# Optimization experiments

Measured on AMD Instinct MI355X. Metric: run time of the kernel, lower is better.

The kernel has to match this reference:

```python
import jax, jax.numpy as jnp
import numpy as np

INNER_STEPS = 50
INNER_LR = 0.1
Y_MEAN = 0.0


def _mlp(params, inp):
    # eqx.nn.MLP(in=3, out=1, width=64, depth=3): relu hidden, identity final
    W1, b1, W2, b2, W3, b3, W4, b4 = params
    h = jax.nn.relu(W1 @ inp + b1)
    h = jax.nn.relu(W2 @ h + b2)
    h = jax.nn.relu(W3 @ h + b3)
    return jnp.squeeze(W4 @ h + b4)


def setup_inputs() -> dict:
    key = jax.random.key(0)
    ks = jax.random.split(key, 10)
    B, CD, W = 8192, 1, 64
    d_in = 2 + CD
    x = jax.random.normal(ks[0], (B, 1), dtype=jnp.float32)
    c = jax.random.normal(ks[1], (B, CD), dtype=jnp.float32)
    def lin(k, fan_out, fan_in):
        lim = 1.0 / np.sqrt(fan_in)
        kw, kb = jax.random.split(k)
        Wm = jax.random.uniform(kw, (fan_out, fan_in), minval=-lim, maxval=lim, dtype=jnp.float32)
        bm = jax.random.uniform(kb, (fan_out,), minval=-lim, maxval=lim, dtype=jnp.float32)
        return Wm, bm
    W1, b1 = lin(ks[2], W, d_in)
    W2, b2 = lin(ks[3], W, W)
    W3, b3 = lin(ks[4], W, W)
    W4, b4 = lin(ks[5], 1, W)
    return {"x": x, "c": c, "W1": W1, "b1": b1, "W2": W2, "b2": b2,
            "W3": W3, "b3": b3, "W4": W4, "b4": b4}


def reference(x, c, W1, b1, W2, b2, W3, b3, W4, b4):
    params = (W1, b1, W2, b2, W3, b3, W4, b4)
    # nearest-neighbor c0 per sample (excluding self)
    dists = jnp.linalg.norm(c[:, None, :] - c[None, :, :], axis=-1)  # [B,B]
    dists = dists + jnp.eye(dists.shape[0], dtype=dists.dtype) * 1e9
    c0 = c[jnp.argmin(dists, axis=1)]  # [B,CD]

    def base_energy(xi, yi, ci):
        return _mlp(params, jnp.concatenate([xi, yi, ci], axis=0))

    def solve(xi, ci, c0i):
        y0 = jnp.array([Y_MEAN], dtype=xi.dtype)

        def step(y, _):
            def loss(yy):
                E0, dE = jax.jvp(lambda cc: base_energy(xi, yy, cc), (c0i,), (ci - c0i,))
                return E0 + dE
            gy = jax.grad(loss)(y)
            return y - INNER_LR * gy, None

        yf, _ = jax.lax.scan(step, y0, None, length=INNER_STEPS)
        return yf

    return jax.vmap(solve)(x, c, c0)  # [B,1]
```

## Files before the change

kernel.cpp:

```cpp
#include <hip/hip_runtime.h>

#define BATCH 8192
#define LOSC  2048.0f
#define LOINV (1.0f / 2048.0f)

typedef _Float16 f16x8 __attribute__((ext_vector_type(8)));
typedef __fp16   fp16x2 __attribute__((ext_vector_type(2)));
typedef float    f32x4 __attribute__((ext_vector_type(4)));

union PK2 { fp16x2 h; unsigned u; };
union U8  { f16x8 v; unsigned u[4]; };

#define FWDMASK 0x00FF00FF00FF00FFULL

__device__ __forceinline__ unsigned pkrtz(float a, float b) {
    PK2 p; p.h = __builtin_amdgcn_cvt_pkrtz(a, b); return p.u;
}

__device__ __forceinline__ unsigned lopair(unsigned hipk, float am, float bm,
                                           float n2048) {
    unsigned d;
    asm("v_fma_mixlo_f16 %0, %1, %2, %3 op_sel:[0,0,0] op_sel_hi:[1,0,0]\n\t"
        "v_fma_mixhi_f16 %0, %1, %2, %4 op_sel:[1,0,0] op_sel_hi:[1,0,0]"
        : "=&v"(d)
        : "v"(hipk), "v"(n2048), "v"(am), "v"(bm));
    return d;
}

__device__ __forceinline__ float xor8f(float v) {
    const int r = __builtin_amdgcn_mov_dpp(__builtin_bit_cast(int, v),
                                           0x128 , 0xf, 0xf, false);
    return __builtin_bit_cast(float, r);
}

__device__ __forceinline__ float selmask(float v, unsigned long long m) {
    float r;
    asm("v_cndmask_b32 %0, 0, %1, %2" : "=v"(r) : "v"(v), "s"(m));
    return r;
}

__device__ __forceinline__ float bfly16(float g) {
    float a = g, b;
    asm volatile("v_mov_b32 %0, %1" : "=v"(b) : "v"(g));
    asm("v_permlane16_swap_b32 %0, %1" : "+v"(a), "+v"(b));
    return a + b;
}
__device__ __forceinline__ float bfly32(float g) {
    float a = g, b;
    asm volatile("v_mov_b32 %0, %1" : "=v"(b) : "v"(g));
    asm("v_permlane32_swap_b32 %0, %1" : "+v"(a), "+v"(b));
    return a + b;
}

__global__ __launch_bounds__(64, 1) void solve_kernel(
    const float* __restrict__ x, const float* __restrict__ c,
    const float* __restrict__ W1, const float* __restrict__ b1,
    const float* __restrict__ W2, const float* __restrict__ b2,
    const float* __restrict__ W3, const float* __restrict__ b3,
    const float* __restrict__ W4, float* __restrict__ out)
{
    const int lane  = threadIdx.x & 63;
    const int sbase = blockIdx.x * 8;
    const float n2048 = -2048.0f;

    __shared__ float cs[BATCH];
    {
        const float4* cg = (const float4*)c;
        float4* cl = (float4*)cs;
        #pragma unroll
        for (int j = 0; j < BATCH / 4 / 64; ++j)
            cl[lane + j * 64] = cg[lane + j * 64];
    }
    __syncthreads();

    float c0s;
    {
        const int g  = lane >> 3;
        const int p  = lane & 7;
        const int si = sbase + g;
        const float ci = cs[si];
        const int sj0 = ((si & 3) == 0) ? (si >> 2) : -1;
        const int sj1 = ((si & 3) == 1) ? (si >> 2) : -1;
        const int sj2 = ((si & 3) == 2) ? (si >> 2) : -1;
        const int sj3 = ((si & 3) == 3) ? (si >> 2) : -1;
        const float4* cs4 = (const float4*)cs;
        float bd0 = 3e38f, bd1 = 3e38f, bd2 = 3e38f, bd3 = 3e38f;
        int   bj0 = 0,     bj1 = 0,     bj2 = 0,     bj3 = 0;
        #pragma unroll 1
        for (int big = 0; big < 16; ++big) {
            float4 vv[16];
            #pragma unroll
            for (int u = 0; u < 16; ++u)
                vv[u] = cs4[p + (big * 16 + u) * 8];
            #pragma unroll
            for (int u = 0; u < 16; ++u) {
                const int jj = p + (big * 16 + u) * 8;
                const float4 v = vv[u];
                float d0 = fabsf(ci - v.x);
                float d1 = fabsf(ci - v.y);
                float d2 = fabsf(ci - v.z);
                float d3 = fabsf(ci - v.w);
                if (jj == sj0) d0 = 3e38f;
                if (jj == sj1) d1 = 3e38f;
                if (jj == sj2) d2 = 3e38f;
                if (jj == sj3) d3 = 3e38f;
                if (d0 < bd0) { bd0 = d0; bj0 = jj; }
                if (d1 < bd1) { bd1 = d1; bj1 = jj; }
                if (d2 < bd2) { bd2 = d2; bj2 = jj; }
                if (d3 < bd3) { bd3 = d3; bj3 = jj; }
            }
        }
        float best = bd0; int bestj = bj0 * 4 + 0;
        { const int j1 = bj1 * 4 + 1; if (bd1 < best || (bd1 == best && j1 < bestj)) { best = bd1; bestj = j1; } }
        { const int j2 = bj2 * 4 + 2; if (bd2 < best || (bd2 == best && j2 < bestj)) { best = bd2; bestj = j2; } }
        { const int j3 = bj3 * 4 + 3; if (bd3 < best || (bd3 == best && j3 < bestj)) { best = bd3; bestj = j3; } }
        #pragma unroll
        for (int off = 1; off < 8; off <<= 1) {
            const float od = __shfl_xor(best, off);
            const int   oj = __shfl_xor(bestj, off);
            if (od < best || (od == best && oj < bestj)) { best = od; bestj = oj; }
        }
        const float bestc = cs[bestj];
        c0s = __shfl(bestc, (lane & 7) << 3);
    }

    const int q  = lane >> 4;
    const int cc = lane & 15;
    const bool fwd = (cc < 8);
    const int s = cc & 7;

    f16x8 W2h[4][2], W2l[4][2], W3h[4][2], W3l[4][2];
    #pragma unroll
    for (int T = 0; T < 4; ++T)
        #pragma unroll
        for (int M = 0; M < 2; ++M) {
            const int off0 = (T * 16 + cc) * 64 + M * 32 + q * 4;
            const int off1 = off0 + 16;
            float4 a = *(const float4*)(W2 + off0);
            float4 b = *(const float4*)(W2 + off1);
            U8 h, l;
            h.u[0] = pkrtz(a.x, a.y); h.u[1] = pkrtz(a.z, a.w);
            h.u[2] = pkrtz(b.x, b.y); h.u[3] = pkrtz(b.z, b.w);
            l.u[0] = lopair(h.u[0], a.x * LOSC, a.y * LOSC, n2048);
            l.u[1] = lopair(h.u[1], a.z * LOSC, a.w * LOSC, n2048);
            l.u[2] = lopair(h.u[2], b.x * LOSC, b.y * LOSC, n2048);
            l.u[3] = lopair(h.u[3], b.z * LOSC, b.w * LOSC, n2048);
            W2h[T][M] = h.v; W2l[T][M] = l.v;
            a = *(const float4*)(W3 + off0);
            b = *(const float4*)(W3 + off1);
            h.u[0] = pkrtz(a.x, a.y); h.u[1] = pkrtz(a.z, a.w);
            h.u[2] = pkrtz(b.x, b.y); h.u[3] = pkrtz(b.z, b.w);
            l.u[0] = lopair(h.u[0], a.x * LOSC, a.y * LOSC, n2048);
            l.u[1] = lopair(h.u[1], a.z * LOSC, a.w * LOSC, n2048);
            l.u[2] = lopair(h.u[2], b.x * LOSC, b.y * LOSC, n2048);
            l.u[3] = lopair(h.u[3], b.z * LOSC, b.w * LOSC, n2048);
            W3h[T][M] = h.v; W3l[T][M] = l.v;
        }

    f32x4 b2q[4], b3q[4];
    const f32x4 zq = {0.f, 0.f, 0.f, 0.f};
    float w4r[16];
    #pragma unroll
    for (int T = 0; T < 4; ++T)
        #pragma unroll
        for (int r = 0; r < 4; ++r) {
            const int row = T * 16 + q * 4 + r;
            b2q[T][r] = fwd ? b2[row] : 0.f;
            b3q[T][r] = fwd ? b3[row] : 0.f;
            w4r[T * 4 + r] = W4[row];
        }

    float A1v[16], w11v[16];
    {
        const float xs = x[sbase + s];
        #pragma unroll
        for (int m = 0; m < 4; ++m)
            #pragma unroll
            for (int j = 0; j < 4; ++j) {
                const int k = m * 16 + q * 4 + j;
                w11v[m * 4 + j] = W1[k * 3 + 1];
                A1v[m * 4 + j]  = fmaf(xs, W1[k * 3 + 0],
                                       fmaf(c0s, W1[k * 3 + 2], b1[k]));
            }
    }

    float y = 0.0f;

    #pragma unroll 1
    for (int step = 0; step < 50; ++step) {
        U8 B1h[2], B1l[2];
        #pragma unroll
        for (int m = 0; m < 4; ++m) {
            float v[4];
            #pragma unroll
            for (int j = 0; j < 4; ++j) {
                const float w = w11v[m * 4 + j];
                const float z = fmaf(y, w, A1v[m * 4 + j]);
                const float a = fwd ? z : w;
                v[j] = (z > 0.f) ? a : 0.f;
            }
            const unsigned h0 = pkrtz(v[0], v[1]);
            const unsigned h1 = pkrtz(v[2], v[3]);
            const int M = m >> 1, o = (m & 1) * 2;
            B1h[M].u[o]     = h0;
            B1h[M].u[o + 1] = h1;
            B1l[M].u[o]     = lopair(h0, v[0] * LOSC, v[1] * LOSC, n2048);
            B1l[M].u[o + 1] = lopair(h1, v[2] * LOSC, v[3] * LOSC, n2048);
        }
        f32x4 ZH[4], ZL[4];
        #pragma unroll
        for (int T = 0; T < 4; ++T) {
            f32x4 aH = __builtin_amdgcn_mfma_f32_16x16x32_f16(W2h[T][0], B1h[0].v, b2q[T], 0, 0, 0);
            f32x4 aL = __builtin_amdgcn_mfma_f32_16x16x32_f16(W2h[T][0], B1l[0].v, zq, 0, 0, 0);
            aL = __builtin_amdgcn_mfma_f32_16x16x32_f16(W2l[T][0], B1h[0].v, aL, 0, 0, 0);
            aH = __builtin_amdgcn_mfma_f32_16x16x32_f16(W2h[T][1], B1h[1].v, aH, 0, 0, 0);
            aL = __builtin_amdgcn_mfma_f32_16x16x32_f16(W2h[T][1], B1l[1].v, aL, 0, 0, 0);
            aL = __builtin_amdgcn_mfma_f32_16x16x32_f16(W2l[T][1], B1h[1].v, aL, 0, 0, 0);
            ZH[T] = aH; ZL[T] = aL;
        }
        {
            float zv[16];
            #pragma unroll
            for (int i = 0; i < 16; ++i)
                zv[i] = fmaf(ZL[i >> 2][i & 3], LOINV, ZH[i >> 2][i & 3]);
            U8 B2h[2], B2l[2];
            #pragma unroll
            for (int T = 0; T < 4; ++T) {
                float v[4];
                #pragma unroll
                for (int r = 0; r < 4; ++r) {
                    const unsigned long long mb = __ballot(zv[T * 4 + r] > 0.f);
                    const unsigned long long t  = mb & FWDMASK;
                    v[r] = selmask(zv[T * 4 + r], t | (t << 8));
                }
                const unsigned h0 = pkrtz(v[0], v[1]);
                const unsigned h1 = pkrtz(v[2], v[3]);
                const int M = T >> 1, o = (T & 1) * 2;
                B2h[M].u[o]     = h0;
                B2h[M].u[o + 1] = h1;
                B2l[M].u[o]     = lopair(h0, v[0] * LOSC, v[1] * LOSC, n2048);
                B2l[M].u[o + 1] = lopair(h1, v[2] * LOSC, v[3] * LOSC, n2048);
            }
            #pragma unroll
            for (int T = 0; T < 4; ++T) {
                f32x4 aH = __builtin_amdgcn_mfma_f32_16x16x32_f16(W3h[T][0], B2h[0].v, b3q[T], 0, 0, 0);
                f32x4 aL = __builtin_amdgcn_mfma_f32_16x16x32_f16(W3h[T][0], B2l[0].v, zq, 0, 0, 0);
                aL = __builtin_amdgcn_mfma_f32_16x16x32_f16(W3l[T][0], B2h[0].v, aL, 0, 0, 0);
                aH = __builtin_amdgcn_mfma_f32_16x16x32_f16(W3h[T][1], B2h[1].v, aH, 0, 0, 0);
                aL = __builtin_amdgcn_mfma_f32_16x16x32_f16(W3h[T][1], B2l[1].v, aL, 0, 0, 0);
                aL = __builtin_amdgcn_mfma_f32_16x16x32_f16(W3l[T][1], B2h[1].v, aL, 0, 0, 0);
                ZH[T] = aH; ZL[T] = aL;
            }
        }
        {
            float zv[16];
            #pragma unroll
            for (int i = 0; i < 16; ++i)
                zv[i] = fmaf(ZL[i >> 2][i & 3], LOINV, ZH[i >> 2][i & 3]);
            float s0 = 0.f, s1 = 0.f, s2 = 0.f, s3 = 0.f;
            #pragma unroll
            for (int T = 0; T < 4; ++T) {
                const int i0 = T * 4;
                const unsigned long long m0 = __ballot(zv[i0 + 0] > 0.f);
                const unsigned long long m1 = __ballot(zv[i0 + 1] > 0.f);
                const unsigned long long m2 = __ballot(zv[i0 + 2] > 0.f);
                const unsigned long long m3 = __ballot(zv[i0 + 3] > 0.f);
                const unsigned long long t0 = m0 & FWDMASK;
                const unsigned long long t1 = m1 & FWDMASK;
                const unsigned long long t2 = m2 & FWDMASK;
                const unsigned long long t3 = m3 & FWDMASK;
                s0 = fmaf(w4r[i0 + 0], selmask(zv[i0 + 0], t0 | (t0 << 8)), s0);
                s1 = fmaf(w4r[i0 + 1], selmask(zv[i0 + 1], t1 | (t1 << 8)), s1);
                s2 = fmaf(w4r[i0 + 2], selmask(zv[i0 + 2], t2 | (t2 << 8)), s2);
                s3 = fmaf(w4r[i0 + 3], selmask(zv[i0 + 3], t3 | (t3 << 8)), s3);
            }
            float g = (s0 + s1) + (s2 + s3);
            g = bfly16(g);
            g = bfly32(g);
            const float gx = xor8f(g);
            g = fwd ? gx : g;
            y -= 0.1f * g;
        }
    }
    if (lane < 8) out[sbase + lane] = y;
}

extern "C" void kernel_launch(void* const* d_in, const int* in_sizes, int n_in,
                              void* d_out, int out_size, void* d_ws, size_t ws_size,
                              hipStream_t stream) {
    const float* x  = (const float*)d_in[0];
    const float* c  = (const float*)d_in[1];
    const float* W1 = (const float*)d_in[2];
    const float* b1 = (const float*)d_in[3];
    const float* W2 = (const float*)d_in[4];
    const float* b2 = (const float*)d_in[5];
    const float* W3 = (const float*)d_in[6];
    const float* b3 = (const float*)d_in[7];
    const float* W4 = (const float*)d_in[8];
    float* out = (float*)d_out;

    solve_kernel<<<BATCH / 8, 64, 0, stream>>>(x, c, W1, b1, W2, b2, W3, b3, W4, out);
}
```

Before: 150.8 us.

## Split MLP hidden rows across two wavefronts per block with LDS exchange

Each block now runs two wavefronts that each own half of the hidden units of layers 2 and 3. Activations and partial gradients are exchanged through shared memory with double-buffered slots and a barrier each half-step. The nearest-neighbour search is also split across 128 threads. The change halves per-wave MFMA work and register pressure and allows more waves per CU, at the cost of two block barriers per inner step and extra LDS traffic on a latency-bound serial loop.

After: 153.2 us. Within noise of the previous version (+1.6%).

```diff
diff --git a/kernel.cpp b/kernel.cpp
--- a/kernel.cpp
+++ b/kernel.cpp
@@ -11,7 +11,7 @@
 union PK2 { fp16x2 h; unsigned u; };
 union U8  { f16x8 v; unsigned u[4]; };
 
-#define FWDMASK 0x00FF00FF00FF00FFULL
+template<int N> struct IC { static constexpr int V = N; };
 
 __device__ __forceinline__ unsigned pkrtz(float a, float b) {
     PK2 p; p.h = __builtin_amdgcn_cvt_pkrtz(a, b); return p.u;
@@ -33,12 +33,6 @@
     return __builtin_bit_cast(float, r);
 }
 
-__device__ __forceinline__ float selmask(float v, unsigned long long m) {
-    float r;
-    asm("v_cndmask_b32 %0, 0, %1, %2" : "=v"(r) : "v"(v), "s"(m));
-    return r;
-}
-
 __device__ __forceinline__ float bfly16(float g) {
     float a = g, b;
     asm volatile("v_mov_b32 %0, %1" : "=v"(b) : "v"(g));
@@ -52,14 +46,16 @@
     return a + b;
 }
 
-__global__ __launch_bounds__(64, 1) void solve_kernel(
+__global__ __launch_bounds__(128, 2) void solve_kernel(
     const float* __restrict__ x, const float* __restrict__ c,
     const float* __restrict__ W1, const float* __restrict__ b1,
     const float* __restrict__ W2, const float* __restrict__ b2,
     const float* __restrict__ W3, const float* __restrict__ b3,
     const float* __restrict__ W4, float* __restrict__ out)
 {
-    const int lane  = threadIdx.x & 63;
+    const int tid   = threadIdx.x;
+    const int wid   = tid >> 6;
+    const int lane  = tid & 63;
     const int sbase = blockIdx.x * 8;
     const float n2048 = -2048.0f;
 
@@ -68,16 +64,16 @@
         const float4* cg = (const float4*)c;
         float4* cl = (float4*)cs;
         #pragma unroll
-        for (int j = 0; j < BATCH / 4 / 64; ++j)
-            cl[lane + j * 64] = cg[lane + j * 64];
+        for (int j = 0; j < BATCH / 4 / 128; ++j)
+            cl[tid + j * 128] = cg[tid + j * 128];
     }
     __syncthreads();
 
     float c0s;
     {
-        const int g  = lane >> 3;
-        const int p  = lane & 7;
-        const int si = sbase + g;
+        const int gs = tid >> 4;
+        const int p  = tid & 15;
+        const int si = sbase + gs;
         const float ci = cs[si];
         const int sj0 = ((si & 3) == 0) ? (si >> 2) : -1;
         const int sj1 = ((si & 3) == 1) ? (si >> 2) : -1;
@@ -87,14 +83,14 @@
         float bd0 = 3e38f, bd1 = 3e38f, bd2 = 3e38f, bd3 = 3e38f;
         int   bj0 = 0,     bj1 = 0,     bj2 = 0,     bj3 = 0;
         #pragma unroll 1
-        for (int big = 0; big < 16; ++big) {
+        for (int big = 0; big < 8; ++big) {
             float4 vv[16];
             #pragma unroll
             for (int u = 0; u < 16; ++u)
-                vv[u] = cs4[p + (big * 16 + u) * 8];
+                vv[u] = cs4[p + (big * 16 + u) * 16];
             #pragma unroll
             for (int u = 0; u < 16; ++u) {
-                const int jj = p + (big * 16 + u) * 8;
+                const int jj = p + (big * 16 + u) * 16;
                 const float4 v = vv[u];
                 float d0 = fabsf(ci - v.x);
                 float d1 = fabsf(ci - v.y);
@@ -115,60 +111,22 @@
         { const int j2 = bj2 * 4 + 2; if (bd2 < best || (bd2 == best && j2 < bestj)) { best = bd2; bestj = j2; } }
         { const int j3 = bj3 * 4 + 3; if (bd3 < best || (bd3 == best && j3 < bestj)) { best = bd3; bestj = j3; } }
         #pragma unroll
-        for (int off = 1; off < 8; off <<= 1) {
+        for (int off = 1; off < 16; off <<= 1) {
             const float od = __shfl_xor(best, off);
             const int   oj = __shfl_xor(bestj, off);
             if (od < best || (od == best && oj < bestj)) { best = od; bestj = oj; }
         }
         const float bestc = cs[bestj];
-        c0s = __shfl(bestc, (lane & 7) << 3);
+        __syncthreads();
+        if (p == 0) cs[gs] = bestc;
+        __syncthreads();
+        c0s = cs[lane & 7];
     }
 
     const int q  = lane >> 4;
     const int cc = lane & 15;
     const bool fwd = (cc < 8);
     const int s = cc & 7;
-
-    f16x8 W2h[4][2], W2l[4][2], W3h[4][2], W3l[4][2];
-    #pragma unroll
-    for (int T = 0; T < 4; ++T)
-        #pragma unroll
-        for (int M = 0; M < 2; ++M) {
-            const int off0 = (T * 16 + cc) * 64 + M * 32 + q * 4;
-            const int off1 = off0 + 16;
-            float4 a = *(const float4*)(W2 + off0);
-            float4 b = *(const float4*)(W2 + off1);
-            U8 h, l;
-            h.u[0] = pkrtz(a.x, a.y); h.u[1] = pkrtz(a.z, a.w);
-            h.u[2] = pkrtz(b.x, b.y); h.u[3] = pkrtz(b.z, b.w);
-            l.u[0] = lopair(h.u[0], a.x * LOSC, a.y * LOSC, n2048);
-            l.u[1] = lopair(h.u[1], a.z * LOSC, a.w * LOSC, n2048);
-            l.u[2] = lopair(h.u[2], b.x * LOSC, b.y * LOSC, n2048);
-            l.u[3] = lopair(h.u[3], b.z * LOSC, b.w * LOSC, n2048);
-            W2h[T][M] = h.v; W2l[T][M] = l.v;
-            a = *(const float4*)(W3 + off0);
-            b = *(const float4*)(W3 + off1);
-            h.u[0] = pkrtz(a.x, a.y); h.u[1] = pkrtz(a.z, a.w);
-            h.u[2] = pkrtz(b.x, b.y); h.u[3] = pkrtz(b.z, b.w);
-            l.u[0] = lopair(h.u[0], a.x * LOSC, a.y * LOSC, n2048);
-            l.u[1] = lopair(h.u[1], a.z * LOSC, a.w * LOSC, n2048);
-            l.u[2] = lopair(h.u[2], b.x * LOSC, b.y * LOSC, n2048);
-            l.u[3] = lopair(h.u[3], b.z * LOSC, b.w * LOSC, n2048);
-            W3h[T][M] = h.v; W3l[T][M] = l.v;
-        }
-
-    f32x4 b2q[4], b3q[4];
-    const f32x4 zq = {0.f, 0.f, 0.f, 0.f};
-    float w4r[16];
-    #pragma unroll
-    for (int T = 0; T < 4; ++T)
-        #pragma unroll
-        for (int r = 0; r < 4; ++r) {
-            const int row = T * 16 + q * 4 + r;
-            b2q[T][r] = fwd ? b2[row] : 0.f;
-            b3q[T][r] = fwd ? b3[row] : 0.f;
-            w4r[T * 4 + r] = W4[row];
-        }
 
     float A1v[16], w11v[16];
     {
@@ -184,105 +142,166 @@
             }
     }
 
-    float y = 0.0f;
-
-    #pragma unroll 1
-    for (int step = 0; step < 50; ++step) {
-        U8 B1h[2], B1l[2];
-        #pragma unroll
-        for (int m = 0; m < 4; ++m) {
-            float v[4];
-            #pragma unroll
-            for (int j = 0; j < 4; ++j) {
-                const float w = w11v[m * 4 + j];
-                const float z = fmaf(y, w, A1v[m * 4 + j]);
-                const float a = fwd ? z : w;
-                v[j] = (z > 0.f) ? a : 0.f;
-            }
-            const unsigned h0 = pkrtz(v[0], v[1]);
-            const unsigned h1 = pkrtz(v[2], v[3]);
-            const int M = m >> 1, o = (m & 1) * 2;
-            B1h[M].u[o]     = h0;
-            B1h[M].u[o + 1] = h1;
-            B1l[M].u[o]     = lopair(h0, v[0] * LOSC, v[1] * LOSC, n2048);
-            B1l[M].u[o + 1] = lopair(h1, v[2] * LOSC, v[3] * LOSC, n2048);
-        }
-        f32x4 ZH[4], ZL[4];
-        #pragma unroll
-        for (int T = 0; T < 4; ++T) {
-            f32x4 aH = __builtin_amdgcn_mfma_f32_16x16x32_f16(W2h[T][0], B1h[0].v, b2q[T], 0, 0, 0);
-            f32x4 aL = __builtin_amdgcn_mfma_f32_16x16x32_f16(W2h[T][0], B1l[0].v, zq, 0, 0, 0);
-            aL = __builtin_amdgcn_mfma_f32_16x16x32_f16(W2l[T][0], B1h[0].v, aL, 0, 0, 0);
-            aH = __builtin_amdgcn_mfma_f32_16x16x32_f16(W2h[T][1], B1h[1].v, aH, 0, 0, 0);
-            aL = __builtin_amdgcn_mfma_f32_16x16x32_f16(W2h[T][1], B1l[1].v, aL, 0, 0, 0);
-            aL = __builtin_amdgcn_mfma_f32_16x16x32_f16(W2l[T][1], B1h[1].v, aL, 0, 0, 0);
-            ZH[T] = aH; ZL[T] = aL;
-        }
-        {
-            float zv[16];
-            #pragma unroll
-            for (int i = 0; i < 16; ++i)
-                zv[i] = fmaf(ZL[i >> 2][i & 3], LOINV, ZH[i >> 2][i & 3]);
-            U8 B2h[2], B2l[2];
-            #pragma unroll
-            for (int T = 0; T < 4; ++T) {
+    f16x8* xb  = (f16x8*)(cs + 16);
+    float* gxb = cs + 2064;
+
+    auto gd = [&](auto wc) {
+        constexpr int WID = decltype(wc)::V;
+
+        f16x8 W2h[2][2], W2l[2][2], W3h[2][2], W3l[2][2];
+        #pragma unroll
+        for (int Tl = 0; Tl < 2; ++Tl)
+            #pragma unroll
+            for (int M = 0; M < 2; ++M) {
+                const int off0 = ((WID * 2 + Tl) * 16 + cc) * 64 + M * 32 + q * 4;
+                const int off1 = off0 + 16;
+                float4 a = *(const float4*)(W2 + off0);
+                float4 b = *(const float4*)(W2 + off1);
+                U8 h, l;
+                h.u[0] = pkrtz(a.x, a.y); h.u[1] = pkrtz(a.z, a.w);
+                h.u[2] = pkrtz(b.x, b.y); h.u[3] = pkrtz(b.z, b.w);
+                l.u[0] = lopair(h.u[0], a.x * LOSC, a.y * LOSC, n2048);
+                l.u[1] = lopair(h.u[1], a.z * LOSC, a.w * LOSC, n2048);
+                l.u[2] = lopair(h.u[2], b.x * LOSC, b.y * LOSC, n2048);
+                l.u[3] = lopair(h.u[3], b.z * LOSC, b.w * LOSC, n2048);
+                W2h[Tl][M] = h.v; W2l[Tl][M] = l.v;
+                a = *(const float4*)(W3 + off0);
+                b = *(const float4*)(W3 + off1);
+                h.u[0] = pkrtz(a.x, a.y); h.u[1] = pkrtz(a.z, a.w);
+                h.u[2] = pkrtz(b.x, b.y); h.u[3] = pkrtz(b.z, b.w);
+                l.u[0] = lopair(h.u[0], a.x * LOSC, a.y * LOSC, n2048);
+                l.u[1] = lopair(h.u[1], a.z * LOSC, a.w * LOSC, n2048);
+                l.u[2] = lopair(h.u[2], b.x * LOSC, b.y * LOSC, n2048);
+                l.u[3] = lopair(h.u[3], b.z * LOSC, b.w * LOSC, n2048);
+                W3h[Tl][M] = h.v; W3l[Tl][M] = l.v;
+            }
+
+        f32x4 b2q[2], b3q[2];
+        const f32x4 zq = {0.f, 0.f, 0.f, 0.f};
+        float w4r[8];
+        #pragma unroll
+        for (int Tl = 0; Tl < 2; ++Tl)
+            #pragma unroll
+            for (int r = 0; r < 4; ++r) {
+                const int row = (WID * 2 + Tl) * 16 + q * 4 + r;
+                b2q[Tl][r] = fwd ? b2[row] : 0.f;
+                b3q[Tl][r] = fwd ? b3[row] : 0.f;
+                w4r[Tl * 4 + r] = W4[row];
+            }
+
+        float y = 0.0f;
+
+        #pragma unroll 1
+        for (int step = 0; step < 50; ++step) {
+            const int par = step & 1;
+            U8 B1h[2], B1l[2];
+            #pragma unroll
+            for (int m = 0; m < 4; ++m) {
                 float v[4];
                 #pragma unroll
-                for (int r = 0; r < 4; ++r) {
-                    const unsigned long long mb = __ballot(zv[T * 4 + r] > 0.f);
-                    const unsigned long long t  = mb & FWDMASK;
-                    v[r] = selmask(zv[T * 4 + r], t | (t << 8));
+                for (int j = 0; j < 4; ++j) {
+                    const float w = w11v[m * 4 + j];
+                    const float z = fmaf(y, w, A1v[m * 4 + j]);
+                    const float a = fwd ? z : w;
+                    v[j] = (z > 0.f) ? a : 0.f;
                 }
                 const unsigned h0 = pkrtz(v[0], v[1]);
                 const unsigned h1 = pkrtz(v[2], v[3]);
-                const int M = T >> 1, o = (T & 1) * 2;
-                B2h[M].u[o]     = h0;
-                B2h[M].u[o + 1] = h1;
-                B2l[M].u[o]     = lopair(h0, v[0] * LOSC, v[1] * LOSC, n2048);
-                B2l[M].u[o + 1] = lopair(h1, v[2] * LOSC, v[3] * LOSC, n2048);
-            }
-            #pragma unroll
-            for (int T = 0; T < 4; ++T) {
-                f32x4 aH = __builtin_amdgcn_mfma_f32_16x16x32_f16(W3h[T][0], B2h[0].v, b3q[T], 0, 0, 0);
-                f32x4 aL = __builtin_amdgcn_mfma_f32_16x16x32_f16(W3h[T][0], B2l[0].v, zq, 0, 0, 0);
-                aL = __builtin_amdgcn_mfma_f32_16x16x32_f16(W3l[T][0], B2h[0].v, aL, 0, 0, 0);
-                aH = __builtin_amdgcn_mfma_f32_16x16x32_f16(W3h[T][1], B2h[1].v, aH, 0, 0, 0);
-                aL = __builtin_amdgcn_mfma_f32_16x16x32_f16(W3h[T][1], B2l[1].v, aL, 0, 0, 0);
-                aL = __builtin_amdgcn_mfma_f32_16x16x32_f16(W3l[T][1], B2h[1].v, aL, 0, 0, 0);
-                ZH[T] = aH; ZL[T] = aL;
-            }
-        }
-        {
-            float zv[16];
-            #pragma unroll
-            for (int i = 0; i < 16; ++i)
-                zv[i] = fmaf(ZL[i >> 2][i & 3], LOINV, ZH[i >> 2][i & 3]);
-            float s0 = 0.f, s1 = 0.f, s2 = 0.f, s3 = 0.f;
-            #pragma unroll
-            for (int T = 0; T < 4; ++T) {
-                const int i0 = T * 4;
-                const unsigned long long m0 = __ballot(zv[i0 + 0] > 0.f);
-                const unsigned long long m1 = __ballot(zv[i0 + 1] > 0.f);
-                const unsigned long long m2 = __ballot(zv[i0 + 2] > 0.f);
-                const unsigned long long m3 = __ballot(zv[i0 + 3] > 0.f);
-                const unsigned long long t0 = m0 & FWDMASK;
-                const unsigned long long t1 = m1 & FWDMASK;
-                const unsigned long long t2 = m2 & FWDMASK;
-                const unsigned long long t3 = m3 & FWDMASK;
-                s0 = fmaf(w4r[i0 + 0], selmask(zv[i0 + 0], t0 | (t0 << 8)), s0);
-                s1 = fmaf(w4r[i0 + 1], selmask(zv[i0 + 1], t1 | (t1 << 8)), s1);
-                s2 = fmaf(w4r[i0 + 2], selmask(zv[i0 + 2], t2 | (t2 << 8)), s2);
-                s3 = fmaf(w4r[i0 + 3], selmask(zv[i0 + 3], t3 | (t3 << 8)), s3);
-            }
-            float g = (s0 + s1) + (s2 + s3);
-            g = bfly16(g);
-            g = bfly32(g);
+                const int M = m >> 1, o = (m & 1) * 2;
+                B1h[M].u[o]     = h0;
+                B1h[M].u[o + 1] = h1;
+                B1l[M].u[o]     = lopair(h0, v[0] * LOSC, v[1] * LOSC, n2048);
+                B1l[M].u[o + 1] = lopair(h1, v[2] * LOSC, v[3] * LOSC, n2048);
+            }
+            f32x4 ZH[2], ZL[2];
+            #pragma unroll
+            for (int Tl = 0; Tl < 2; ++Tl) {
+                f32x4 aH = __builtin_amdgcn_mfma_f32_16x16x32_f16(W2h[Tl][0], B1h[0].v, b2q[Tl], 0, 0, 0);
+                f32x4 aL = __builtin_amdgcn_mfma_f32_16x16x32_f16(W2h[Tl][0], B1l[0].v, zq, 0, 0, 0);
+                aL = __builtin_amdgcn_mfma_f32_16x16x32_f16(W2l[Tl][0], B1h[0].v, aL, 0, 0, 0);
+                aH = __builtin_amdgcn_mfma_f32_16x16x32_f16(W2h[Tl][1], B1h[1].v, aH, 0, 0, 0);
+                aL = __builtin_amdgcn_mfma_f32_16x16x32_f16(W2h[Tl][1], B1l[1].v, aL, 0, 0, 0);
+                aL = __builtin_amdgcn_mfma_f32_16x16x32_f16(W2l[Tl][1], B1h[1].v, aL, 0, 0, 0);
+                ZH[Tl] = aH; ZL[Tl] = aL;
+            }
+            U8 oh, ol;
+            {
+                float zv[8], rv[8];
+                #pragma unroll
+                for (int i = 0; i < 8; ++i)
+                    zv[i] = fmaf(ZL[i >> 2][i & 3], LOINV, ZH[i >> 2][i & 3]);
+                #pragma unroll
+                for (int i = 0; i < 8; ++i)
+                    rv[i] = xor8f(zv[i]);
+                #pragma unroll
+                for (int Tl = 0; Tl < 2; ++Tl) {
+                    float v[4];
+                    #pragma unroll
+                    for (int r = 0; r < 4; ++r) {
+                        const float z = zv[Tl * 4 + r];
+                        const float gate = fwd ? z : rv[Tl * 4 + r];
+                        v[r] = (gate > 0.f) ? z : 0.f;
+                    }
+                    const unsigned h0 = pkrtz(v[0], v[1]);
+                    const unsigned h1 = pkrtz(v[2], v[3]);
+                    oh.u[Tl * 2]     = h0;
+                    oh.u[Tl * 2 + 1] = h1;
+                    ol.u[Tl * 2]     = lopair(h0, v[0] * LOSC, v[1] * LOSC, n2048);
+                    ol.u[Tl * 2 + 1] = lopair(h1, v[2] * LOSC, v[3] * LOSC, n2048);
+                }
+            }
+            xb[((par * 2 + WID) * 2 + 0) * 64 + lane] = oh.v;
+            xb[((par * 2 + WID) * 2 + 1) * 64 + lane] = ol.v;
+            __syncthreads();
+            const f16x8 ph = xb[((par * 2 + (WID ^ 1)) * 2 + 0) * 64 + lane];
+            const f16x8 pl = xb[((par * 2 + (WID ^ 1)) * 2 + 1) * 64 + lane];
+            f16x8 B2h0, B2l0, B2h1, B2l1;
+            if constexpr (WID == 0) { B2h0 = oh.v; B2l0 = ol.v; B2h1 = ph; B2l1 = pl; }
+            else                    { B2h0 = ph;   B2l0 = pl;   B2h1 = oh.v; B2l1 = ol.v; }
+            #pragma unroll
+            for (int Tl = 0; Tl < 2; ++Tl) {
+                f32x4 aH = __builtin_amdgcn_mfma_f32_16x16x32_f16(W3h[Tl][0], B2h0, b3q[Tl], 0, 0, 0);
+                f32x4 aL = __builtin_amdgcn_mfma_f32_16x16x32_f16(W3h[Tl][0], B2l0, zq, 0, 0, 0);
+                aL = __builtin_amdgcn_mfma_f32_16x16x32_f16(W3l[Tl][0], B2h0, aL, 0, 0, 0);
+                aH = __builtin_amdgcn_mfma_f32_16x16x32_f16(W3h[Tl][1], B2h1, aH, 0, 0, 0);
+                aL = __builtin_amdgcn_mfma_f32_16x16x32_f16(W3h[Tl][1], B2l1, aL, 0, 0, 0);
+                aL = __builtin_amdgcn_mfma_f32_16x16x32_f16(W3l[Tl][1], B2h1, aL, 0, 0, 0);
+                ZH[Tl] = aH; ZL[Tl] = aL;
+            }
+            float gp;
+            {
+                float zv[8], rv[8];
+                #pragma unroll
+                for (int i = 0; i < 8; ++i)
+                    zv[i] = fmaf(ZL[i >> 2][i & 3], LOINV, ZH[i >> 2][i & 3]);
+                #pragma unroll
+                for (int i = 0; i < 8; ++i)
+                    rv[i] = xor8f(zv[i]);
+                float s0 = 0.f, s1 = 0.f;
+                #pragma unroll
+                for (int r = 0; r < 4; ++r) {
+                    const float ga = fwd ? zv[r] : rv[r];
+                    const float va = fwd ? rv[r] : zv[r];
+                    s0 = fmaf(w4r[r], (ga > 0.f) ? va : 0.f, s0);
+                    const float gb = fwd ? zv[4 + r] : rv[4 + r];
+                    const float vb = fwd ? rv[4 + r] : zv[4 + r];
+                    s1 = fmaf(w4r[4 + r], (gb > 0.f) ? vb : 0.f, s1);
+                }
+                gp = s0 + s1;
+                gp = bfly16(gp);
+                gp = bfly32(gp);
+            }
+            gxb[(par * 2 + WID) * 64 + lane] = gp;
+            __syncthreads();
+            float g = gp + gxb[(par * 2 + (WID ^ 1)) * 64 + lane];
             const float gx = xor8f(g);
             g = fwd ? gx : g;
             y -= 0.1f * g;
         }
-    }
-    if (lane < 8) out[sbase + lane] = y;
+        if (WID == 0 && lane < 8) out[sbase + lane] = y;
+    };
+
+    if (wid == 0) gd(IC<0>{}); else gd(IC<1>{});
 }
 
 extern "C" void kernel_launch(void* const* d_in, const int* in_sizes, int n_in,
@@ -299,5 +318,5 @@
     const float* W4 = (const float*)d_in[8];
     float* out = (float*)d_out;
 
-    solve_kernel<<<BATCH / 8, 64, 0, stream>>>(x, c, W1, b1, W2, b2, W3, b3, W4, out);
-}
+    solve_kernel<<<BATCH / 8, 128, 0, stream>>>(x, c, W1, b1, W2, b2, W3, b3, W4, out);
+}
```
